# Performance work log

Measured on AMD Instinct MI355X. Metric: run time of the kernel, lower is better.

The kernel has to match this reference:

```python
import jax, jax.numpy as jnp
import numpy as np

L = 6        # num_coupling_layers
T_DIM = 64   # t_dim
HALF = T_DIM // 2
COND = 128   # cond_dim
HID = 1024   # hidden_dim
B = 32768


def setup_inputs() -> dict:
    key = jax.random.key(0)
    ks = jax.random.split(key, 8)
    s_in = 1.0 / np.sqrt(HALF + COND)
    s_h = 1.0 / np.sqrt(HID)
    T = jax.random.normal(ks[0], (B, T_DIM), dtype=jnp.float32)
    cond = jax.random.normal(ks[1], (B, COND), dtype=jnp.float32)
    W1 = jax.random.normal(ks[2], (L, HALF + COND, HID), dtype=jnp.float32) * s_in
    b1 = jnp.zeros((L, HID), dtype=jnp.float32)
    W2 = jax.random.normal(ks[3], (L, HID, HID), dtype=jnp.float32) * s_h
    b2 = jnp.zeros((L, HID), dtype=jnp.float32)
    W3 = jax.random.normal(ks[4], (L, HID, 2 * HALF), dtype=jnp.float32) * s_h
    b3 = jnp.zeros((L, 2 * HALF), dtype=jnp.float32)
    return {"T": T, "cond": cond, "W1": W1, "b1": b1, "W2": W2, "b2": b2, "W3": W3, "b3": b3}


def reference(T, cond, W1, b1, W2, b2, W3, b3):
    # Conditional normalizing flow: 6 affine coupling layers with alternating
    # contiguous half masks. Even layers transform the first half, odd the second.
    def mlp(h, i):
        x = jax.nn.relu(h @ W1[i] + b1[i])
        x = jax.nn.relu(x @ W2[i] + b2[i])
        return x @ W3[i] + b3[i]

    z = T
    log_det = jnp.zeros(T.shape[0], dtype=T.dtype)
    for i in range(L):
        if i % 2 == 0:
            masked, unmasked = z[:, :HALF], z[:, HALF:]
        else:
            masked, unmasked = z[:, HALF:], z[:, :HALF]
        params = mlp(jnp.concatenate([unmasked, cond], axis=1), i)
        s = jnp.tanh(params[:, :HALF])
        t_shift = params[:, HALF:]
        y_masked = masked * jnp.exp(s) + t_shift
        if i % 2 == 0:
            z = jnp.concatenate([y_masked, unmasked], axis=1)
        else:
            z = jnp.concatenate([unmasked, y_masked], axis=1)
        log_det = log_det + jnp.sum(s, axis=1)
    return z, log_det
```

## Files before the change

### kernel.cpp

```cpp
#include <hip/hip_runtime.h>
#include <hip/hip_fp16.h>
#include <stdint.h>

typedef _Float16 f16;
typedef _Float16 f16x8 __attribute__((ext_vector_type(8)));
typedef float f32x4 __attribute__((ext_vector_type(4)));

#define NB 32768
#define LAYERS 6
#define AK 160
#define HID 1024

__device__ __forceinline__ void async_copy16(const void* g, void* l) {
  __builtin_amdgcn_global_load_lds(
      (const __attribute__((address_space(1))) void*)g,
      (__attribute__((address_space(3))) void*)l, 16, 0, 0);
}

__device__ __forceinline__ void wtrans_tile(const float* __restrict__ W,
                                            f16* __restrict__ Wt,
                                            const int K_, const int N_,
                                            const int bx, const int by,
                                            const int bz, float (*t)[65])
{
  const long off = (long)bz * K_ * N_;
  const float* Wl = W + off;
  f16* Wtl = Wt + off;
  const int k0 = by * 64, n0 = bx * 64;
  const int tx = threadIdx.x & 63, ty4 = threadIdx.x >> 6;
#pragma unroll
  for (int r = ty4; r < 64; r += 4) {
    const int k = k0 + r;
    if (k < K_) t[r][tx] = Wl[(long)k * N_ + n0 + tx];
  }
  __syncthreads();
  const int k = k0 + tx;
  if (k < K_) {
#pragma unroll
    for (int r = ty4; r < 64; r += 4) {
      const int n = n0 + r;
      Wtl[(long)n * K_ + k] = (f16)t[tx][r];
    }
  }
}

__global__ void prep_all(const float* __restrict__ T, const float* __restrict__ cond,
                         const float* __restrict__ W1, const float* __restrict__ W2,
                         const float* __restrict__ W3,
                         float* __restrict__ z, float* __restrict__ ld,
                         f16* __restrict__ A,
                         f16* __restrict__ W1t, f16* __restrict__ W2t,
                         f16* __restrict__ W3t)
{
  __shared__ float t[64][65];
  const int b = blockIdx.x;
  if (b < 2048) {
    const int S1 = NB * 64;
    const int S2 = S1 + NB;
    const int S3 = S2 + NB * 32;
    const int S4 = S3 + NB * 128;
    for (int i = b * blockDim.x + threadIdx.x; i < S4; i += 2048 * blockDim.x) {
      if (i < S1) {
        z[i] = T[i];
      } else if (i < S2) {
        ld[i - S1] = 0.0f;
      } else if (i < S3) {
        int r = i - S2;
        int row = r >> 5, j = r & 31;
        A[(size_t)row * AK + j] = (f16)T[row * 64 + 32 + j];
      } else {
        int r = i - S3;
        int row = r >> 7, j = r & 127;
        A[(size_t)row * AK + 32 + j] = (f16)cond[r];
      }
    }
  } else if (b < 2048 + 288) {
    const int l = b - 2048;
    wtrans_tile(W1, W1t, AK, 1024, l % 16, (l / 16) % 3, l / 48, t);
  } else if (b < 2048 + 288 + 1536) {
    const int l = b - (2048 + 288);
    wtrans_tile(W2, W2t, HID, 1024, l % 16, (l / 16) % 16, l / 256, t);
  } else {
    const int l = b - (2048 + 288 + 1536);
    wtrans_tile(W3, W3t, HID, 64, 0, l % 16, l / 16, t);
  }
}

__global__ __launch_bounds__(256, 2)
void gemm1_full(const f16* __restrict__ A,
                const f16* __restrict__ Wt,
                const float* __restrict__ bias,
                f16* __restrict__ C)
{
  __shared__ __align__(16) f16 As[128 * 160];
  __shared__ __align__(16) f16 Bs[128 * 160];
  const int tid  = threadIdx.x;
  const int lane = tid & 63;
  const int wave = tid >> 6;
  const int c15  = lane & 15;
  const int quad = lane >> 4;
  const int wm = (wave & 1) * 64;
  const int wn = (wave >> 1) * 64;

  const int b = blockIdx.x;
  const int x = b & 7, i = b >> 3;
  const long rowStart = (long)(x * 32 + (i >> 3)) * 128;
  const long colStart = (long)(i & 7) * 128;

  const f16* Ab = A  + rowStart * AK;
  const f16* Bb = Wt + colStart * AK;

#pragma unroll
  for (int it = 0; it < 10; ++it) {
    const int f = it * 256 + tid;
    const int row = f / 20;
    const int ch  = f - row * 20;
    const int chs = ch ^ ((row >> 1) & 3);
    async_copy16(Ab + (long)row * AK + chs * 8, &As[0] + (long)f * 8);
    async_copy16(Bb + (long)row * AK + chs * 8, &Bs[0] + (long)f * 8);
  }
  __syncthreads();

  f32x4 acc[4][4] = {};
#pragma unroll
  for (int kt = 0; kt < 5; ++kt) {
    f16x8 a[4], bf[4];
#pragma unroll
    for (int mi = 0; mi < 4; ++mi) {
      const int R = wm + mi * 16 + c15;
      a[mi] = *(const f16x8*)&As[(R * 20 + kt * 4 + (quad ^ ((R >> 1) & 3))) * 8];
    }
#pragma unroll
    for (int ni = 0; ni < 4; ++ni) {
      const int R = wn + ni * 16 + c15;
      bf[ni] = *(const f16x8*)&Bs[(R * 20 + kt * 4 + (quad ^ ((R >> 1) & 3))) * 8];
    }
#pragma unroll
    for (int mi = 0; mi < 4; ++mi)
#pragma unroll
      for (int ni = 0; ni < 4; ++ni)
        acc[mi][ni] = __builtin_amdgcn_mfma_f32_16x16x32_f16(
            a[mi], bf[ni], acc[mi][ni], 0, 0, 0);
  }

#pragma unroll
  for (int ni = 0; ni < 4; ++ni) {
    const long gn = colStart + wn + ni * 16 + c15;
    const float bv = bias[gn];
#pragma unroll
    for (int mi = 0; mi < 4; ++mi) {
#pragma unroll
      for (int r = 0; r < 4; ++r) {
        const long gm = rowStart + wm + mi * 16 + quad * 4 + r;
        float v = acc[mi][ni][r] + bv;
        v = fmaxf(v, 0.0f);
        C[gm * HID + gn] = (f16)v;
      }
    }
  }
}

__global__ __launch_bounds__(256, 3)
void gemm12(const f16* __restrict__ A, const int K,
            const f16* __restrict__ Wt,
            const float* __restrict__ bias,
            f16* __restrict__ C)
{
  __shared__ __align__(16) f16 As[2][128 * 32];
  __shared__ __align__(16) f16 Bs[2][128 * 32];
  const int tid  = threadIdx.x;
  const int wave = tid >> 6;
  const int lane = tid & 63;
  const int c15  = lane & 15;
  const int quad = lane >> 4;
  const int wm = (wave & 1) * 64;
  const int wn = (wave >> 1) * 64;

  const int b = blockIdx.x;
  const int x = b & 7, i = b >> 3;
  const long rowStart = (long)(x * 32 + (i >> 3)) * 128;
  const long colStart = (long)(i & 7) * 128;

  const f16* Ab = A  + rowStart * K;
  const f16* Bb = Wt + colStart * K;

  const int ra  = tid >> 2;
  const int kca = (((tid & 3) ^ ((ra >> 1) & 3))) * 8;

  f32x4 acc[4][4] = {};
  const int nK = K >> 5;

  auto stage = [&](int kt, int sel) {
    const long ko = (long)kt * 32;
    f16* as = &As[sel][0];
    f16* bs = &Bs[sel][0];
#pragma unroll
    for (int q = 0; q < 2; ++q)
      async_copy16(Ab + (long)(q * 64 + ra) * K + ko + kca,
                   as + (q * 256 + wave * 64) * 8);
#pragma unroll
    for (int q = 0; q < 2; ++q)
      async_copy16(Bb + (long)(q * 64 + ra) * K + ko + kca,
                   bs + (q * 256 + wave * 64) * 8);
  };

  stage(0, 0);
  for (int kt = 0; kt < nK; ++kt) {
    __syncthreads();
    if (kt + 1 < nK) stage(kt + 1, (kt + 1) & 1);
    const f16* as = &As[kt & 1][0];
    const f16* bs = &Bs[kt & 1][0];

    f16x8 a[4], bf[4];
#pragma unroll
    for (int mi = 0; mi < 4; ++mi) {
      const int R = wm + mi * 16 + c15;
      a[mi] = *(const f16x8*)&as[R * 32 + ((quad ^ ((R >> 1) & 3)) << 3)];
    }
#pragma unroll
    for (int ni = 0; ni < 4; ++ni) {
      const int R = wn + ni * 16 + c15;
      bf[ni] = *(const f16x8*)&bs[R * 32 + ((quad ^ ((R >> 1) & 3)) << 3)];
    }
#pragma unroll
    for (int mi = 0; mi < 4; ++mi)
#pragma unroll
      for (int ni = 0; ni < 4; ++ni)
        acc[mi][ni] = __builtin_amdgcn_mfma_f32_16x16x32_f16(
            a[mi], bf[ni], acc[mi][ni], 0, 0, 0);
  }

#pragma unroll
  for (int ni = 0; ni < 4; ++ni) {
    const long gn = colStart + wn + ni * 16 + c15;
    const float bv = bias[gn];
#pragma unroll
    for (int mi = 0; mi < 4; ++mi) {
#pragma unroll
      for (int r = 0; r < 4; ++r) {
        const long gm = rowStart + wm + mi * 16 + quad * 4 + r;
        float v = acc[mi][ni][r] + bv;
        v = fmaxf(v, 0.0f);
        C[gm * HID + gn] = (f16)v;
      }
    }
  }
}

__global__ __launch_bounds__(256, 2)
void gemm3_coupling(const f16* __restrict__ X2, const f16* __restrict__ W3t,
                    const float* __restrict__ b3, float* __restrict__ z,
                    float* __restrict__ log_det, f16* __restrict__ Anext,
                    const int maskoff)
{
  __shared__ __align__(16) f16 As[2][64 * 64];
  __shared__ __align__(16) f16 Bs[2][64 * 64];
  const int tid = threadIdx.x;
  const int wave = tid >> 6, lane = tid & 63;
  const int c15 = lane & 15, quad = lane >> 4;
  const int wm = wave * 16;
  const long rowStart = (long)blockIdx.x * 64;

  const f16* Ab = X2 + rowStart * HID;
  const int brow = tid >> 3;
  const int bkc  = ((tid & 7) ^ (brow & 7)) * 8;

  f32x4 acc[4] = {};

  auto stage = [&](int c, int sel) {
    const long kb = (long)c * 64;
#pragma unroll
    for (int q = 0; q < 2; ++q) {
      async_copy16(Ab  + (long)(q * 32 + brow) * HID + kb + bkc,
                   &As[sel][0] + (q * 256 + wave * 64) * 8);
      async_copy16(W3t + (long)(q * 32 + brow) * HID + kb + bkc,
                   &Bs[sel][0] + (q * 256 + wave * 64) * 8);
    }
  };

  stage(0, 0);
  for (int c = 0; c < 16; ++c) {
    __syncthreads();
    if (c + 1 < 16) stage(c + 1, (c + 1) & 1);
    const f16* as = &As[c & 1][0];
    const f16* bs = &Bs[c & 1][0];

#pragma unroll
    for (int s = 0; s < 2; ++s) {
      const int Ra = wm + c15;
      f16x8 a = *(const f16x8*)&as[(Ra * 8 + ((s * 4 + quad) ^ (Ra & 7))) * 8];
      f16x8 bf[4];
#pragma unroll
      for (int ni = 0; ni < 4; ++ni) {
        const int R = ni * 16 + c15;
        bf[ni] = *(const f16x8*)&bs[(R * 8 + ((s * 4 + quad) ^ (R & 7))) * 8];
      }
#pragma unroll
      for (int ni = 0; ni < 4; ++ni)
        acc[ni] = __builtin_amdgcn_mfma_f32_16x16x32_f16(a, bf[ni], acc[ni], 0, 0, 0);
    }
  }

  float sp[4] = {0.0f, 0.0f, 0.0f, 0.0f};
#pragma unroll
  for (int ni = 0; ni < 2; ++ni) {
    const int j = ni * 16 + c15;
    const float bs = b3[j];
    const float bt = b3[32 + j];
#pragma unroll
    for (int r = 0; r < 4; ++r) {
      const long gm = rowStart + wm + quad * 4 + r;
      const float sv = acc[ni][r] + bs;
      const float e2 = __expf(2.0f * sv);
      const float s  = 1.0f - 2.0f / (e2 + 1.0f);
      const float tv = acc[ni + 2][r] + bt;
      const float m  = z[gm * 64 + maskoff + j];
      const float y  = fmaf(m, __expf(s), tv);
      z[gm * 64 + maskoff + j] = y;
      Anext[gm * AK + j] = (f16)y;
      sp[r] += s;
    }
  }
#pragma unroll
  for (int r = 0; r < 4; ++r) {
    float v = sp[r];
    v += __shfl_xor(v, 1);
    v += __shfl_xor(v, 2);
    v += __shfl_xor(v, 4);
    v += __shfl_xor(v, 8);
    if (c15 == 0) {
      const long gm = rowStart + wm + quad * 4 + r;
      log_det[gm] += v;
    }
  }
}

extern "C" void kernel_launch(void* const* d_in, const int* in_sizes, int n_in,
                              void* d_out, int out_size, void* d_ws, size_t ws_size,
                              hipStream_t stream) {
  (void)in_sizes; (void)n_in; (void)out_size; (void)ws_size;
  const float* T    = (const float*)d_in[0];
  const float* cond = (const float*)d_in[1];
  const float* W1   = (const float*)d_in[2];
  const float* b1   = (const float*)d_in[3];
  const float* W2   = (const float*)d_in[4];
  const float* b2   = (const float*)d_in[5];
  const float* W3   = (const float*)d_in[6];
  const float* b3   = (const float*)d_in[7];

  float* z  = (float*)d_out;
  float* ld = z + (size_t)NB * 64;

  f16* A   = (f16*)d_ws;
  f16* X1  = A   + (size_t)NB * AK;
  f16* X2  = X1  + (size_t)NB * HID;
  f16* W1t = X2  + (size_t)NB * HID;
  f16* W2t = W1t + (size_t)6 * 1024 * 160;
  f16* W3t = W2t + ((size_t)6 << 20);

  prep_all<<<3968, 256, 0, stream>>>(T, cond, W1, W2, W3,
                                     z, ld, A, W1t, W2t, W3t);

  const int g12 = (NB / 128) * (HID / 128);
  for (int l = 0; l < LAYERS; ++l) {
    gemm1_full<<<g12, 256, 0, stream>>>(A, W1t + (size_t)l * 1024 * AK,
                                        b1 + l * 1024, X1);
    gemm12<<<g12, 256, 0, stream>>>(X1, HID, W2t + ((size_t)l << 20),
                                    b2 + l * 1024, X2);
    const int maskoff = (l & 1) ? 32 : 0;
    gemm3_coupling<<<NB / 64, 256, 0, stream>>>(X2, W3t + (size_t)l * 64 * 1024,
                                                b3 + l * 64, z, ld, A, maskoff);
  }
}
```

Before: 855.1 us.

## Replace hidden GEMM with 256x256-tile, 8-wave, phased pipelined kernel

The 1024x1024 hidden-layer GEMM moves from 128x128 tiles with 4 waves and K=32 steps to 256x256 tiles with 8 waves and K=64 steps. Each K step is split into four MFMA phases that interleave half-tile async global-to-LDS loads with compute, using s_setprio and explicit waitcnt/barriers to overlap transfers and math. The larger tiles cut global and LDS traffic per FLOP. In exchange the kernel uses 128 KB of LDS per block and many more accumulator registers, which limits occupancy, and it depends on hand-tuned vmcnt counts being correct.

New measurement: 813.6 us. -4.9%, faster.

```diff
diff --git a/kernel.cpp b/kernel.cpp
--- a/kernel.cpp
+++ b/kernel.cpp
@@ -160,88 +160,181 @@
   }
 }
 
-__global__ __launch_bounds__(256, 3)
-void gemm12(const f16* __restrict__ A, const int K,
-            const f16* __restrict__ Wt,
-            const float* __restrict__ bias,
-            f16* __restrict__ C)
+__global__ __launch_bounds__(512, 2)
+void gemm2_8ph(const f16* __restrict__ A,
+               const f16* __restrict__ Wt,
+               const float* __restrict__ bias,
+               f16* __restrict__ C)
 {
-  __shared__ __align__(16) f16 As[2][128 * 32];
-  __shared__ __align__(16) f16 Bs[2][128 * 32];
+  __shared__ __align__(16) f16 As[2][16384];
+  __shared__ __align__(16) f16 Bs[2][16384];
+
   const int tid  = threadIdx.x;
+  const int lane = tid & 63;
   const int wave = tid >> 6;
-  const int lane = tid & 63;
   const int c15  = lane & 15;
   const int quad = lane >> 4;
-  const int wm = (wave & 1) * 64;
-  const int wn = (wave >> 1) * 64;
+  const int wm = (wave >> 2) * 128;
+  const int wn = (wave & 3) * 64;
 
   const int b = blockIdx.x;
-  const int x = b & 7, i = b >> 3;
-  const long rowStart = (long)(x * 32 + (i >> 3)) * 128;
-  const long colStart = (long)(i & 7) * 128;
-
-  const f16* Ab = A  + rowStart * K;
-  const f16* Bb = Wt + colStart * K;
-
-  const int ra  = tid >> 2;
-  const int kca = (((tid & 3) ^ ((ra >> 1) & 3))) * 8;
-
-  f32x4 acc[4][4] = {};
-  const int nK = K >> 5;
-
-  auto stage = [&](int kt, int sel) {
-    const long ko = (long)kt * 32;
-    f16* as = &As[sel][0];
-    f16* bs = &Bs[sel][0];
-#pragma unroll
-    for (int q = 0; q < 2; ++q)
-      async_copy16(Ab + (long)(q * 64 + ra) * K + ko + kca,
-                   as + (q * 256 + wave * 64) * 8);
-#pragma unroll
-    for (int q = 0; q < 2; ++q)
-      async_copy16(Bb + (long)(q * 64 + ra) * K + ko + kca,
-                   bs + (q * 256 + wave * 64) * 8);
+  const int wgid = (b & 7) * 64 + (b >> 3);
+  const long rowStart = (long)(wgid >> 2) * 256;
+  const long colStart = (long)(wgid & 3) * 256;
+
+  const f16* Ab = A  + rowStart * HID;
+  const f16* Bb = Wt + colStart * HID;
+
+  const int rh0 = tid >> 3,        ch0 = tid & 7;
+  const int rh1 = 64 + (tid >> 3), ch1 = tid & 7;
+  const long g0 = (long)rh0 * HID + ((ch0 ^ (rh0 & 7)) << 3);
+  const long g1 = (long)rh1 * HID + ((ch1 ^ (rh1 & 7)) << 3);
+  const int l0 = tid << 3;
+  const int l1 = (512 + tid) << 3;
+
+  auto stageA = [&](int kt2, int h, int sel) {
+    const f16* src = Ab + (long)h * 128 * HID + (long)kt2 * 64;
+    f16* dst = &As[sel][h * 8192];
+    async_copy16(src + g0, dst + l0);
+    async_copy16(src + g1, dst + l1);
   };
-
-  stage(0, 0);
-  for (int kt = 0; kt < nK; ++kt) {
-    __syncthreads();
-    if (kt + 1 < nK) stage(kt + 1, (kt + 1) & 1);
-    const f16* as = &As[kt & 1][0];
-    const f16* bs = &Bs[kt & 1][0];
-
-    f16x8 a[4], bf[4];
+  auto stageB = [&](int kt2, int h, int sel) {
+    const f16* src = Bb + (long)h * 128 * HID + (long)kt2 * 64;
+    f16* dst = &Bs[sel][h * 8192];
+    async_copy16(src + g0, dst + l0);
+    async_copy16(src + g1, dst + l1);
+  };
+
+  stageA(0, 0, 0); stageA(0, 1, 0);
+  stageB(0, 0, 0); stageB(0, 1, 0);
+  stageB(1, 0, 1); stageA(1, 0, 1);
+  asm volatile("s_waitcnt vmcnt(4)" ::: "memory");
+  __builtin_amdgcn_s_barrier();
+  __builtin_amdgcn_sched_barrier(0);
+
+  f32x4 acc[8][4] = {};
+
+#pragma unroll 2
+  for (int kt = 0; kt < 16; ++kt) {
+    const int sel = kt & 1;
+    const f16* as = &As[sel][0];
+    const f16* bs = &Bs[sel][0];
+    const bool s1 = (kt + 1 < 16);
+    const bool s2 = (kt + 2 < 16);
+    f16x8 a0[4][2], a1[4][2], b0[2][2], b1[2][2];
+
 #pragma unroll
     for (int mi = 0; mi < 4; ++mi) {
-      const int R = wm + mi * 16 + c15;
-      a[mi] = *(const f16x8*)&as[R * 32 + ((quad ^ ((R >> 1) & 3)) << 3)];
-    }
-#pragma unroll
-    for (int ni = 0; ni < 4; ++ni) {
-      const int R = wn + ni * 16 + c15;
-      bf[ni] = *(const f16x8*)&bs[R * 32 + ((quad ^ ((R >> 1) & 3)) << 3)];
-    }
+      const int r = wm + mi * 16 + c15;
+#pragma unroll
+      for (int ks = 0; ks < 2; ++ks)
+        a0[mi][ks] = *(const f16x8*)&as[r * 64 + ((((ks << 2) + quad) ^ (r & 7)) << 3)];
+    }
+#pragma unroll
+    for (int ni = 0; ni < 2; ++ni) {
+      const int r = wn + ni * 16 + c15;
+#pragma unroll
+      for (int ks = 0; ks < 2; ++ks)
+        b0[ni][ks] = *(const f16x8*)&bs[r * 64 + ((((ks << 2) + quad) ^ (r & 7)) << 3)];
+    }
+    if (s1) stageA(kt + 1, 1, sel ^ 1);
+    __builtin_amdgcn_s_barrier();
+    asm volatile("s_waitcnt lgkmcnt(0)" ::: "memory");
+    __builtin_amdgcn_sched_barrier(0);
+    __builtin_amdgcn_s_setprio(1);
 #pragma unroll
     for (int mi = 0; mi < 4; ++mi)
 #pragma unroll
-      for (int ni = 0; ni < 4; ++ni)
-        acc[mi][ni] = __builtin_amdgcn_mfma_f32_16x16x32_f16(
-            a[mi], bf[ni], acc[mi][ni], 0, 0, 0);
-  }
-
-#pragma unroll
-  for (int ni = 0; ni < 4; ++ni) {
-    const long gn = colStart + wn + ni * 16 + c15;
+      for (int ni = 0; ni < 2; ++ni)
+#pragma unroll
+        for (int ks = 0; ks < 2; ++ks)
+          acc[mi][ni] = __builtin_amdgcn_mfma_f32_16x16x32_f16(
+              a0[mi][ks], b0[ni][ks], acc[mi][ni], 0, 0, 0);
+    __builtin_amdgcn_s_setprio(0);
+    __builtin_amdgcn_sched_barrier(0);
+    __builtin_amdgcn_s_barrier();
+
+#pragma unroll
+    for (int ni = 0; ni < 2; ++ni) {
+      const int r = wn + 32 + ni * 16 + c15;
+#pragma unroll
+      for (int ks = 0; ks < 2; ++ks)
+        b1[ni][ks] = *(const f16x8*)&bs[r * 64 + ((((ks << 2) + quad) ^ (r & 7)) << 3)];
+    }
+    if (s1) stageB(kt + 1, 1, sel ^ 1);
+    __builtin_amdgcn_s_barrier();
+    asm volatile("s_waitcnt lgkmcnt(0)" ::: "memory");
+    __builtin_amdgcn_sched_barrier(0);
+    __builtin_amdgcn_s_setprio(1);
+#pragma unroll
+    for (int mi = 0; mi < 4; ++mi)
+#pragma unroll
+      for (int ni = 0; ni < 2; ++ni)
+#pragma unroll
+        for (int ks = 0; ks < 2; ++ks)
+          acc[mi][2 + ni] = __builtin_amdgcn_mfma_f32_16x16x32_f16(
+              a0[mi][ks], b1[ni][ks], acc[mi][2 + ni], 0, 0, 0);
+    __builtin_amdgcn_s_setprio(0);
+    __builtin_amdgcn_sched_barrier(0);
+    __builtin_amdgcn_s_barrier();
+
+#pragma unroll
+    for (int mi = 0; mi < 4; ++mi) {
+      const int r = wm + 64 + mi * 16 + c15;
+#pragma unroll
+      for (int ks = 0; ks < 2; ++ks)
+        a1[mi][ks] = *(const f16x8*)&as[r * 64 + ((((ks << 2) + quad) ^ (r & 7)) << 3)];
+    }
+    if (s2) stageB(kt + 2, 0, sel);
+    __builtin_amdgcn_s_barrier();
+    asm volatile("s_waitcnt lgkmcnt(0)" ::: "memory");
+    __builtin_amdgcn_sched_barrier(0);
+    __builtin_amdgcn_s_setprio(1);
+#pragma unroll
+    for (int mi = 0; mi < 4; ++mi)
+#pragma unroll
+      for (int ni = 0; ni < 2; ++ni)
+#pragma unroll
+        for (int ks = 0; ks < 2; ++ks)
+          acc[4 + mi][ni] = __builtin_amdgcn_mfma_f32_16x16x32_f16(
+              a1[mi][ks], b0[ni][ks], acc[4 + mi][ni], 0, 0, 0);
+    __builtin_amdgcn_s_setprio(0);
+    __builtin_amdgcn_sched_barrier(0);
+    __builtin_amdgcn_s_barrier();
+
+    if (s2) stageA(kt + 2, 0, sel);
+    __builtin_amdgcn_s_setprio(1);
+#pragma unroll
+    for (int mi = 0; mi < 4; ++mi)
+#pragma unroll
+      for (int ni = 0; ni < 2; ++ni)
+#pragma unroll
+        for (int ks = 0; ks < 2; ++ks)
+          acc[4 + mi][2 + ni] = __builtin_amdgcn_mfma_f32_16x16x32_f16(
+              a1[mi][ks], b1[ni][ks], acc[4 + mi][2 + ni], 0, 0, 0);
+    __builtin_amdgcn_s_setprio(0);
+    if (s2) {
+      asm volatile("s_waitcnt vmcnt(4)" ::: "memory");
+    } else if (s1) {
+      asm volatile("s_waitcnt vmcnt(0)" ::: "memory");
+    }
+    __builtin_amdgcn_sched_barrier(0);
+    __builtin_amdgcn_s_barrier();
+  }
+
+#pragma unroll
+  for (int nii = 0; nii < 4; ++nii) {
+    const int nof = (nii >> 1) * 32 + (nii & 1) * 16;
+    const long gn = colStart + wn + nof + c15;
     const float bv = bias[gn];
 #pragma unroll
-    for (int mi = 0; mi < 4; ++mi) {
+    for (int mii = 0; mii < 8; ++mii) {
+      const int mof = (mii >> 2) * 64 + (mii & 3) * 16;
 #pragma unroll
       for (int r = 0; r < 4; ++r) {
-        const long gm = rowStart + wm + mi * 16 + quad * 4 + r;
-        float v = acc[mi][ni][r] + bv;
-        v = fmaxf(v, 0.0f);
-        C[gm * HID + gn] = (f16)v;
+        const long gm = rowStart + wm + mof + quad * 4 + r;
+        float v = acc[mii][nii][r] + bv;
+        C[gm * HID + gn] = (f16)fmaxf(v, 0.0f);
       }
     }
   }
@@ -361,12 +454,13 @@
   prep_all<<<3968, 256, 0, stream>>>(T, cond, W1, W2, W3,
                                      z, ld, A, W1t, W2t, W3t);
 
-  const int g12 = (NB / 128) * (HID / 128);
+  const int g1 = (NB / 128) * (HID / 128);
+  const int g2 = (NB / 256) * (HID / 256);
   for (int l = 0; l < LAYERS; ++l) {
-    gemm1_full<<<g12, 256, 0, stream>>>(A, W1t + (size_t)l * 1024 * AK,
-                                        b1 + l * 1024, X1);
-    gemm12<<<g12, 256, 0, stream>>>(X1, HID, W2t + ((size_t)l << 20),
-                                    b2 + l * 1024, X2);
+    gemm1_full<<<g1, 256, 0, stream>>>(A, W1t + (size_t)l * 1024 * AK,
+                                       b1 + l * 1024, X1);
+    gemm2_8ph<<<g2, 512, 0, stream>>>(X1, W2t + ((size_t)l << 20),
+                                      b2 + l * 1024, X2);
     const int maskoff = (l & 1) ? 32 : 0;
     gemm3_coupling<<<NB / 64, 256, 0, stream>>>(X2, W3t + (size_t)l * 64 * 1024,
                                                 b3 + l * 64, z, ld, A, maskoff);
```

## Replace hidden-layer GEMM with 256x256-tile 8-wave kernel and explicit pipelining

Applied to the files above, without the earlier changes.

The 1024x1024 hidden GEMM kernel is replaced by one that computes a 256x256 output tile per 512-thread workgroup. Each wave now holds an 8x4 grid of MFMA accumulators, which raises operand reuse from shared memory and cuts global traffic per FLOP. The K loop is restructured with manual waitcnt/barrier placement, prefetch two stages ahead into double buffers, and raised wave priority around the MFMA block to overlap loads with compute. The larger accumulator footprint increases register pressure and there are fewer workgroups for the 256 CUs. The early-iteration buffer reuse also relies on the hand-placed barriers being correct.

New measurement: 811.5 us. 1.05x faster.

```diff
diff --git a/kernel.cpp b/kernel.cpp
--- a/kernel.cpp
+++ b/kernel.cpp
@@ -160,88 +160,101 @@
   }
 }
 
-__global__ __launch_bounds__(256, 3)
-void gemm12(const f16* __restrict__ A, const int K,
-            const f16* __restrict__ Wt,
-            const float* __restrict__ bias,
-            f16* __restrict__ C)
-{
-  __shared__ __align__(16) f16 As[2][128 * 32];
-  __shared__ __align__(16) f16 Bs[2][128 * 32];
+__global__ __launch_bounds__(512, 2)
+void gemm2_sp(const f16* __restrict__ A,
+              const f16* __restrict__ Wt,
+              const float* __restrict__ bias,
+              f16* __restrict__ C)
+{
+  __shared__ __align__(16) f16 As[2][8192];
+  __shared__ __align__(16) f16 Bs[2][8192];
+
   const int tid  = threadIdx.x;
+  const int lane = tid & 63;
   const int wave = tid >> 6;
-  const int lane = tid & 63;
   const int c15  = lane & 15;
   const int quad = lane >> 4;
-  const int wm = (wave & 1) * 64;
-  const int wn = (wave >> 1) * 64;
+  const int wm = (wave >> 2) * 128;
+  const int wn = (wave & 3) * 64;
 
   const int b = blockIdx.x;
-  const int x = b & 7, i = b >> 3;
-  const long rowStart = (long)(x * 32 + (i >> 3)) * 128;
-  const long colStart = (long)(i & 7) * 128;
-
-  const f16* Ab = A  + rowStart * K;
-  const f16* Bb = Wt + colStart * K;
-
-  const int ra  = tid >> 2;
-  const int kca = (((tid & 3) ^ ((ra >> 1) & 3))) * 8;
-
-  f32x4 acc[4][4] = {};
-  const int nK = K >> 5;
-
-  auto stage = [&](int kt, int sel) {
-    const long ko = (long)kt * 32;
-    f16* as = &As[sel][0];
-    f16* bs = &Bs[sel][0];
-#pragma unroll
-    for (int q = 0; q < 2; ++q)
-      async_copy16(Ab + (long)(q * 64 + ra) * K + ko + kca,
-                   as + (q * 256 + wave * 64) * 8);
-#pragma unroll
-    for (int q = 0; q < 2; ++q)
-      async_copy16(Bb + (long)(q * 64 + ra) * K + ko + kca,
-                   bs + (q * 256 + wave * 64) * 8);
+  const int wgid = (b & 7) * 64 + (b >> 3);
+  const long rowStart = (long)(wgid >> 2) * 256;
+  const long colStart = (long)(wgid & 3) * 256;
+
+  const f16* Ab = A  + rowStart * HID;
+  const f16* Bb = Wt + colStart * HID;
+
+  const int r0  = tid >> 2;
+  const int ch0 = tid & 3;
+  const long g0 = (long)r0 * HID + (((ch0 ^ ((r0 >> 1) & 3))) << 3);
+  const int l0 = tid << 3;
+
+  auto stageFull = [&](int kt2, int sel) {
+    const f16* sa = Ab + (long)kt2 * 32;
+    const f16* sb = Bb + (long)kt2 * 32;
+    f16* da = &As[sel][0];
+    f16* db = &Bs[sel][0];
+    async_copy16(sa + g0,                  da + l0);
+    async_copy16(sa + (long)128 * HID + g0, da + 4096 + l0);
+    async_copy16(sb + g0,                  db + l0);
+    async_copy16(sb + (long)128 * HID + g0, db + 4096 + l0);
   };
 
-  stage(0, 0);
-  for (int kt = 0; kt < nK; ++kt) {
-    __syncthreads();
-    if (kt + 1 < nK) stage(kt + 1, (kt + 1) & 1);
-    const f16* as = &As[kt & 1][0];
-    const f16* bs = &Bs[kt & 1][0];
-
-    f16x8 a[4], bf[4];
-#pragma unroll
-    for (int mi = 0; mi < 4; ++mi) {
-      const int R = wm + mi * 16 + c15;
-      a[mi] = *(const f16x8*)&as[R * 32 + ((quad ^ ((R >> 1) & 3)) << 3)];
-    }
-#pragma unroll
-    for (int ni = 0; ni < 4; ++ni) {
-      const int R = wn + ni * 16 + c15;
-      bf[ni] = *(const f16x8*)&bs[R * 32 + ((quad ^ ((R >> 1) & 3)) << 3)];
-    }
-#pragma unroll
-    for (int mi = 0; mi < 4; ++mi)
-#pragma unroll
-      for (int ni = 0; ni < 4; ++ni)
-        acc[mi][ni] = __builtin_amdgcn_mfma_f32_16x16x32_f16(
-            a[mi], bf[ni], acc[mi][ni], 0, 0, 0);
-  }
-
-#pragma unroll
-  for (int ni = 0; ni < 4; ++ni) {
-    const long gn = colStart + wn + ni * 16 + c15;
+  stageFull(0, 0);
+  stageFull(1, 1);
+  asm volatile("s_waitcnt vmcnt(4)" ::: "memory");
+  __builtin_amdgcn_s_barrier();
+  __builtin_amdgcn_sched_barrier(0);
+
+  f32x4 acc[8][4] = {};
+
+#pragma unroll 2
+  for (int kt = 0; kt < 32; ++kt) {
+    const int sel = kt & 1;
+    const f16* as = &As[sel][0];
+    const f16* bs = &Bs[sel][0];
+    const int ktp2 = (kt + 2 < 32) ? kt + 2 : 31;
+
+    f16x8 a[8], bf[4];
+#pragma unroll
+    for (int m = 0; m < 8; ++m) {
+      const int r = wm + m * 16 + c15;
+      a[m] = *(const f16x8*)&as[r * 32 + ((quad ^ ((r >> 1) & 3)) << 3)];
+    }
+#pragma unroll
+    for (int n = 0; n < 4; ++n) {
+      const int r = wn + n * 16 + c15;
+      bf[n] = *(const f16x8*)&bs[r * 32 + ((quad ^ ((r >> 1) & 3)) << 3)];
+    }
+    asm volatile("s_waitcnt lgkmcnt(0)" ::: "memory");
+    __builtin_amdgcn_s_barrier();
+    stageFull(ktp2, sel);
+    __builtin_amdgcn_sched_barrier(0);
+    __builtin_amdgcn_s_setprio(1);
+#pragma unroll
+    for (int m = 0; m < 8; ++m)
+#pragma unroll
+      for (int n = 0; n < 4; ++n)
+        acc[m][n] = __builtin_amdgcn_mfma_f32_16x16x32_f16(
+            a[m], bf[n], acc[m][n], 0, 0, 0);
+    __builtin_amdgcn_s_setprio(0);
+    __builtin_amdgcn_sched_barrier(0);
+    asm volatile("s_waitcnt vmcnt(4)" ::: "memory");
+    __builtin_amdgcn_s_barrier();
+  }
+
+#pragma unroll
+  for (int n = 0; n < 4; ++n) {
+    const long gn = colStart + wn + n * 16 + c15;
     const float bv = bias[gn];
 #pragma unroll
-    for (int mi = 0; mi < 4; ++mi) {
+    for (int m = 0; m < 8; ++m) {
 #pragma unroll
       for (int r = 0; r < 4; ++r) {
-        const long gm = rowStart + wm + mi * 16 + quad * 4 + r;
-        float v = acc[mi][ni][r] + bv;
-        v = fmaxf(v, 0.0f);
-        C[gm * HID + gn] = (f16)v;
+        const long gm = rowStart + wm + m * 16 + quad * 4 + r;
+        float v = acc[m][n][r] + bv;
+        C[gm * HID + gn] = (f16)fmaxf(v, 0.0f);
       }
     }
   }
@@ -361,12 +374,13 @@
   prep_all<<<3968, 256, 0, stream>>>(T, cond, W1, W2, W3,
                                      z, ld, A, W1t, W2t, W3t);
 
-  const int g12 = (NB / 128) * (HID / 128);
+  const int g1 = (NB / 128) * (HID / 128);
+  const int g2 = (NB / 256) * (HID / 256);
   for (int l = 0; l < LAYERS; ++l) {
-    gemm1_full<<<g12, 256, 0, stream>>>(A, W1t + (size_t)l * 1024 * AK,
-                                        b1 + l * 1024, X1);
-    gemm12<<<g12, 256, 0, stream>>>(X1, HID, W2t + ((size_t)l << 20),
-                                    b2 + l * 1024, X2);
+    gemm1_full<<<g1, 256, 0, stream>>>(A, W1t + (size_t)l * 1024 * AK,
+                                       b1 + l * 1024, X1);
+    gemm2_sp<<<g2, 512, 0, stream>>>(X1, W2t + ((size_t)l << 20),
+                                     b2 + l * 1024, X2);
     const int maskoff = (l & 1) ? 32 : 0;
     gemm3_coupling<<<NB / 64, 256, 0, stream>>>(X2, W3t + (size_t)l * 64 * 1024,
                                                 b3 + l * 64, z, ld, A, maskoff);
```
